# Optimization experiments

Measured on AMD Instinct MI355X. Metric: run time of the kernel, lower is better.

Reference implementation:

```python
import jax, jax.numpy as jnp
import numpy as np

V, E, H, O, L = 32000, 512, 512, 32, 2
B, T = 64, 512


def setup_inputs() -> dict:
    key = jax.random.key(0)
    ks = jax.random.split(key, 10)
    s = 0.02
    x = jax.random.randint(ks[0], (B, T), 0, V, dtype=jnp.int64)
    seq_lens = jax.random.randint(ks[1], (B,), 1, T + 1, dtype=jnp.int64)
    emb = jax.random.normal(ks[2], (V, E), dtype=jnp.float32) * s
    Whx = jax.random.normal(ks[3], (L, H, E), dtype=jnp.float32) * s  # [out,in] like nn.Linear
    Whh = jax.random.normal(ks[4], (L, H, H), dtype=jnp.float32) * s
    b_h = jnp.zeros((L, H), dtype=jnp.float32)
    Wyh = jax.random.normal(ks[5], (L, H, H), dtype=jnp.float32) * s
    b_y = jnp.zeros((L, H), dtype=jnp.float32)
    Wf = jax.random.normal(ks[6], (O, H), dtype=jnp.float32) * s
    bf = jnp.zeros((O,), dtype=jnp.float32)
    return {"x": x, "sequence_lengths": seq_lens, "emb": emb, "Whx": Whx,
            "Whh": Whh, "b_h": b_h, "Wyh": Wyh, "b_y": b_y, "Wf": Wf, "bf": bf}


def reference(x, sequence_lengths, emb, Whx, Whh, b_h, Wyh, b_y, Wf, bf):
    Bsz, Tlen = x.shape
    x_emb = emb[x]                      # [B,T,E]
    xs = jnp.swapaxes(x_emb, 0, 1)      # time-major [T,B,E]
    h0 = jnp.zeros((L, Bsz, H), dtype=x_emb.dtype)

    def step(h, xt):
        inp = xt
        hs = []
        for l in range(L):
            hl = jnp.tanh(inp @ Whx[l].T + h[l] @ Whh[l].T + b_h[l])
            hs.append(hl)
            inp = hl
        # only the last layer's y is kept by the original loop
        y = inp @ Wyh[L - 1].T + b_y[L - 1]
        return jnp.stack(hs), y

    _, outputs = jax.lax.scan(step, h0, xs)     # outputs: [T,B,H]
    outputs = jnp.swapaxes(outputs, 0, 1)       # [B,T,H]
    idx = sequence_lengths - 1                  # last valid timestep per example
    final_hidden = outputs[jnp.arange(Bsz), idx]  # [B,H]
    return final_hidden @ Wf.T + bf             # [B,O]
```

## Files before the change

kernel.cpp:

```cpp
#include <hip/hip_runtime.h>

namespace {
constexpr int E_ = 512;
constexpr int H_ = 512;
constexpr int O_ = 32;
constexpr int B_ = 64;
constexpr int T_ = 512;
constexpr int RING = 8;
constexpr int FPAD = 16;
constexpr size_t H0_OFF   = 0;
constexpr size_t H1_OFF   = (size_t)RING * B_ * H_;
constexpr size_t HF_OFF   = 2 * H1_OFF;
constexpr size_t FLAG_OFF = HF_OFF + (size_t)B_ * H_;
constexpr size_t FLAG_UINTS = 2u * 8u * 32u * FPAD;
constexpr size_t WS_REQUIRED = (FLAG_OFF + FLAG_UINTS) * 4;
}

typedef float f32x4 __attribute__((ext_vector_type(4)));

__device__ __forceinline__ void coh_ld2k(const float* p, f32x4& a, f32x4& b) {
    asm volatile(
        "global_load_dwordx4 %0, %2, off sc0 sc1\n\t"
        "global_load_dwordx4 %1, %2, off offset:1024 sc0 sc1\n\t"
        "s_waitcnt vmcnt(0)"
        : "=&v"(a), "=&v"(b) : "v"(p) : "memory");
}
__device__ __forceinline__ void coh_ld4k(const float* p, const float* q,
                                         f32x4& a, f32x4& b, f32x4& c, f32x4& d) {
    asm volatile(
        "global_load_dwordx4 %0, %4, off sc0 sc1\n\t"
        "global_load_dwordx4 %1, %4, off offset:1024 sc0 sc1\n\t"
        "global_load_dwordx4 %2, %5, off sc0 sc1\n\t"
        "global_load_dwordx4 %3, %5, off offset:1024 sc0 sc1\n\t"
        "s_waitcnt vmcnt(0)"
        : "=&v"(a), "=&v"(b), "=&v"(c), "=&v"(d) : "v"(p), "v"(q) : "memory");
}
__device__ __forceinline__ unsigned flag_poll(const unsigned* p) {
    unsigned v;
    asm volatile("global_load_dword %0, %1, off sc0 sc1\n\ts_waitcnt vmcnt(0)"
                 : "=&v"(v) : "v"(p) : "memory");
    return v;
}
__device__ __forceinline__ void vm_drain() {
    asm volatile("s_waitcnt vmcnt(0)" ::: "memory");
}
__device__ __forceinline__ void coh_store(float* p, float v) {
    asm volatile("global_store_dword %0, %1, off sc0 sc1" :: "v"(p), "v"(v) : "memory");
}
__device__ __forceinline__ void flag_store(unsigned* p, unsigned v) {
    asm volatile("global_store_dword %0, %1, off sc0 sc1" :: "v"(p), "v"(v) : "memory");
}

__device__ __forceinline__ float fast_tanh(float x) {
    float e = __builtin_amdgcn_exp2f(x * 2.885390081777927f);
    return 1.0f - 2.0f * __builtin_amdgcn_rcpf(e + 1.0f);
}

__device__ __forceinline__ float reduce4(const float v[4], int lane) {
    float a[2];
#pragma unroll
    for (int j = 0; j < 2; ++j) {
        const int sel = lane & 1;
        const float mine = sel ? v[2 * j + 1] : v[2 * j];
        const float send = sel ? v[2 * j] : v[2 * j + 1];
        a[j] = mine + __shfl_xor(send, 1, 64);
    }
    const int sel = (lane >> 1) & 1;
    const float mine = sel ? a[1] : a[0];
    const float send = sel ? a[0] : a[1];
    float s = mine + __shfl_xor(send, 2, 64);
    s += __shfl_xor(s, 4, 64);
    s += __shfl_xor(s, 8, 64);
    s += __shfl_xor(s, 16, 64);
    s += __shfl_xor(s, 32, 64);
    return s;
}

__global__ __launch_bounds__(512, 4) void rnn_pipe8(
    const int* __restrict__ x, const int* __restrict__ seq_lens,
    const float* __restrict__ emb,
    const float* __restrict__ Whx, const float* __restrict__ Whh,
    const float* __restrict__ b_h,
    float* __restrict__ h0_ring, float* __restrict__ h1_ring,
    float* __restrict__ h1_final, unsigned* __restrict__ flags)
{
    const int bid   = blockIdx.x;
    const int layer = bid >> 8;
    const int g     = (bid >> 5) & 7;
    const int c     = bid & 31;
    const int tid   = threadIdx.x;
    const int wid   = tid >> 6;
    const int lane  = tid & 63;
    const int we    = wid >> 2;
    const int wr    = wid & 3;
    const int rowbase = c * 16 + wr * 4;
    const int eg0   = g * 8 + we * 4;

    __shared__ float sx[2][4096];
    __shared__ float sh[4096];
    __shared__ float sh1[4096];

    const float* WxL = Whx + (size_t)layer * H_ * E_;
    const float* WhL = Whh + (size_t)layer * H_ * H_;
    f32x4 wx0[4], wx1[4], wh0[4], wh1[4];
#pragma unroll
    for (int r = 0; r < 4; ++r) {
        const int row = rowbase + r;
        wx0[r] = *(const f32x4*)(WxL + (size_t)row * E_ + (lane << 2));
        wx1[r] = *(const f32x4*)(WxL + (size_t)row * E_ + 256 + (lane << 2));
        wh0[r] = *(const f32x4*)(WhL + (size_t)row * H_ + (lane << 2));
        wh1[r] = *(const f32x4*)(WhL + (size_t)row * H_ + 256 + (lane << 2));
    }
    const float bias = b_h[layer * H_ + rowbase + (lane & 3)];

    int sl4[4];
#pragma unroll
    for (int q = 0; q < 4; ++q) sl4[q] = seq_lens[eg0 + q];
    int Tg = 1;
#pragma unroll
    for (int j = 0; j < 8; ++j) {
        const int s = seq_lens[g * 8 + j];
        Tg = s > Tg ? s : Tg;
    }

    unsigned* const myflag = flags + ((size_t)((layer * 8 + g) * 32 + c)) * FPAD;
    const unsigned* const pollp = (lane < 32)
        ? flags + ((size_t)(g * 32 + lane)) * FPAD
        : flags + ((size_t)((8 + g) * 32 + (lane - 32))) * FPAD;

    const int se  = wid;
    const int seg = g * 8 + se;

    long budget = 1l << 24;

    if (layer == 0) {
        {
            const int tok = x[(size_t)seg * T_];
            *(f32x4*)&sx[0][(se << 9) + (lane << 2)] =
                *(const f32x4*)(emb + ((size_t)tok << 9) + (lane << 2));
            *(f32x4*)&sx[0][(se << 9) + 256 + (lane << 2)] =
                *(const f32x4*)(emb + ((size_t)tok << 9) + 256 + (lane << 2));
        }
        __syncthreads();

        for (int t = 0; t < Tg; ++t) {
            const int cur = t & 1, slot = t & 7, pslot = (t - 1) & 7;
            float vvp[4][4];

#pragma unroll
            for (int q = 0; q < 4; ++q) {
                if (t >= sl4[q]) continue;
                const int el = (we << 2) + q;
                const f32x4 lx0 = *(const f32x4*)&sx[cur][(el << 9) + (lane << 2)];
                const f32x4 lx1 = *(const f32x4*)&sx[cur][(el << 9) + 256 + (lane << 2)];
#pragma unroll
                for (int r = 0; r < 4; ++r) {
                    float s = wx0[r][0] * lx0[0];
                    s = fmaf(wx0[r][1], lx0[1], s);
                    s = fmaf(wx0[r][2], lx0[2], s);
                    s = fmaf(wx0[r][3], lx0[3], s);
                    s = fmaf(wx1[r][0], lx1[0], s);
                    s = fmaf(wx1[r][1], lx1[1], s);
                    s = fmaf(wx1[r][2], lx1[2], s);
                    s = fmaf(wx1[r][3], lx1[3], s);
                    vvp[q][r] = s;
                }
            }
            f32x4 px0, px1;
            const bool havepf = (t + 1 < Tg);
            if (havepf) {
                const int tok = x[(size_t)seg * T_ + t + 1];
                px0 = *(const f32x4*)(emb + ((size_t)tok << 9) + (lane << 2));
                px1 = *(const f32x4*)(emb + ((size_t)tok << 9) + 256 + (lane << 2));
            }
            if (wid == 0 && t > 0) {
                const int tgt = (lane < 32) ? t : t - 7;
                for (;;) {
                    const unsigned v = flag_poll(pollp);
                    if (!__any((int)v < tgt)) break;
                    if (--budget < 0) break;
                }
            }
            __syncthreads();

            if (t > 0) {
                f32x4 a, b;
                coh_ld2k(h0_ring + (((size_t)pslot << 6) + seg) * 512 + (lane << 2), a, b);
                *(f32x4*)&sh[(se << 9) + (lane << 2)] = a;
                *(f32x4*)&sh[(se << 9) + 256 + (lane << 2)] = b;
            } else {
                f32x4 z = 0;
                *(f32x4*)&sh[(se << 9) + (lane << 2)] = z;
                *(f32x4*)&sh[(se << 9) + 256 + (lane << 2)] = z;
            }
            __syncthreads();

#pragma unroll
            for (int q = 0; q < 4; ++q) {
                if (t >= sl4[q]) continue;
                const int el = (we << 2) + q;
                const f32x4 h0a = *(const f32x4*)&sh[(el << 9) + (lane << 2)];
                const f32x4 h0b = *(const f32x4*)&sh[(el << 9) + 256 + (lane << 2)];
#pragma unroll
                for (int r = 0; r < 4; ++r) {
                    float s = vvp[q][r];
                    s = fmaf(wh0[r][0], h0a[0], s);
                    s = fmaf(wh0[r][1], h0a[1], s);
                    s = fmaf(wh0[r][2], h0a[2], s);
                    s = fmaf(wh0[r][3], h0a[3], s);
                    s = fmaf(wh1[r][0], h0b[0], s);
                    s = fmaf(wh1[r][1], h0b[1], s);
                    s = fmaf(wh1[r][2], h0b[2], s);
                    s = fmaf(wh1[r][3], h0b[3], s);
                    vvp[q][r] = s;
                }
                const float sum = reduce4(vvp[q], lane);
                const float hv = fast_tanh(sum + bias);
                if (lane < 4)
                    coh_store(h0_ring + (((size_t)slot << 6) + eg0 + q) * 512 + rowbase + lane, hv);
            }
            if (havepf) {
                *(f32x4*)&sx[cur ^ 1][(se << 9) + (lane << 2)] = px0;
                *(f32x4*)&sx[cur ^ 1][(se << 9) + 256 + (lane << 2)] = px1;
            }
            vm_drain();
            __syncthreads();
            if (tid == 0) flag_store(myflag, (unsigned)(t + 1));
        }
    } else {
        for (int t = 0; t < Tg; ++t) {
            const int slot = t & 7, pslot = (t - 1) & 7;
            float vvp[4][4];

            if (wid == 0) {
                const int tgt = (lane < 32) ? t + 1 : t;
                for (;;) {
                    const unsigned v = flag_poll(pollp);
                    if (!__any((int)v < tgt)) break;
                    if (--budget < 0) break;
                }
            }
            __syncthreads();

            if (t > 0) {
                f32x4 a, b, cc, d;
                coh_ld4k(h0_ring + (((size_t)slot << 6) + seg) * 512 + (lane << 2),
                         h1_ring + (((size_t)pslot << 6) + seg) * 512 + (lane << 2),
                         a, b, cc, d);
                *(f32x4*)&sh[(se << 9) + (lane << 2)] = a;
                *(f32x4*)&sh[(se << 9) + 256 + (lane << 2)] = b;
                *(f32x4*)&sh1[(se << 9) + (lane << 2)] = cc;
                *(f32x4*)&sh1[(se << 9) + 256 + (lane << 2)] = d;
            } else {
                f32x4 a, b;
                coh_ld2k(h0_ring + (((size_t)slot << 6) + seg) * 512 + (lane << 2), a, b);
                *(f32x4*)&sh[(se << 9) + (lane << 2)] = a;
                *(f32x4*)&sh[(se << 9) + 256 + (lane << 2)] = b;
                f32x4 z = 0;
                *(f32x4*)&sh1[(se << 9) + (lane << 2)] = z;
                *(f32x4*)&sh1[(se << 9) + 256 + (lane << 2)] = z;
            }
            __syncthreads();

#pragma unroll
            for (int q = 0; q < 4; ++q) {
                if (t >= sl4[q]) continue;
                const int el = (we << 2) + q;
                const f32x4 xa = *(const f32x4*)&sh[(el << 9) + (lane << 2)];
                const f32x4 xb = *(const f32x4*)&sh[(el << 9) + 256 + (lane << 2)];
                const f32x4 ha = *(const f32x4*)&sh1[(el << 9) + (lane << 2)];
                const f32x4 hb = *(const f32x4*)&sh1[(el << 9) + 256 + (lane << 2)];
#pragma unroll
                for (int r = 0; r < 4; ++r) {
                    float s = wx0[r][0] * xa[0];
                    s = fmaf(wx0[r][1], xa[1], s);
                    s = fmaf(wx0[r][2], xa[2], s);
                    s = fmaf(wx0[r][3], xa[3], s);
                    s = fmaf(wx1[r][0], xb[0], s);
                    s = fmaf(wx1[r][1], xb[1], s);
                    s = fmaf(wx1[r][2], xb[2], s);
                    s = fmaf(wx1[r][3], xb[3], s);
                    s = fmaf(wh0[r][0], ha[0], s);
                    s = fmaf(wh0[r][1], ha[1], s);
                    s = fmaf(wh0[r][2], ha[2], s);
                    s = fmaf(wh0[r][3], ha[3], s);
                    s = fmaf(wh1[r][0], hb[0], s);
                    s = fmaf(wh1[r][1], hb[1], s);
                    s = fmaf(wh1[r][2], hb[2], s);
                    s = fmaf(wh1[r][3], hb[3], s);
                    vvp[q][r] = s;
                }
                const float sum = reduce4(vvp[q], lane);
                const float hv = fast_tanh(sum + bias);
                if (lane < 4) {
                    coh_store(h1_ring + (((size_t)slot << 6) + eg0 + q) * 512 + rowbase + lane, hv);
                    if (t == sl4[q] - 1)
                        h1_final[((size_t)(eg0 + q) << 9) + rowbase + lane] = hv;
                }
            }
            vm_drain();
            __syncthreads();
            if (tid == 0) flag_store(myflag, (unsigned)(t + 1));
        }
    }
}

__device__ __forceinline__ float dot4(float4 a, float4 b) {
    return fmaf(a.x, b.x, fmaf(a.y, b.y, fmaf(a.z, b.z, a.w * b.w)));
}
__device__ __forceinline__ float wave_reduce(float acc) {
#pragma unroll
    for (int off = 32; off > 0; off >>= 1) acc += __shfl_down(acc, off, 64);
    return acc;
}

__global__ __launch_bounds__(512) void head_kernel(
    const float* __restrict__ h1f, const float* __restrict__ Wyh,
    const float* __restrict__ b_y, const float* __restrict__ Wf,
    const float* __restrict__ bf, float* __restrict__ out)
{
    const int e = blockIdx.x;
    const int tid = threadIdx.x, wid = tid >> 6, lane = tid & 63;
    const int k0 = lane << 3;
    __shared__ float sh[H_];
    __shared__ float sy[H_];
    sh[tid] = h1f[(size_t)e * H_ + tid];
    __syncthreads();
    const float4 hA = *(const float4*)&sh[k0];
    const float4 hB = *(const float4*)&sh[k0 + 4];
    const float* Wy1 = Wyh + H_ * H_;
#pragma unroll 4
    for (int rr = 0; rr < 64; ++rr) {
        const int row = (wid << 6) + rr;
        float acc = wave_reduce(dot4(*(const float4*)&Wy1[(size_t)row * H_ + k0], hA) +
                                dot4(*(const float4*)&Wy1[(size_t)row * H_ + k0 + 4], hB));
        if (lane == 0) sy[row] = acc + b_y[H_ + row];
    }
    __syncthreads();
    const float4 yA = *(const float4*)&sy[k0];
    const float4 yB = *(const float4*)&sy[k0 + 4];
#pragma unroll
    for (int rr = 0; rr < 4; ++rr) {
        const int o = (wid << 2) + rr;
        float acc = wave_reduce(dot4(*(const float4*)&Wf[(size_t)o * H_ + k0], yA) +
                                dot4(*(const float4*)&Wf[(size_t)o * H_ + k0 + 4], yB));
        if (lane == 0) out[(size_t)e * O_ + o] = acc + bf[o];
    }
}

__global__ __launch_bounds__(1024, 1) void rnn_fused_fb(
    const int* __restrict__ x, const int* __restrict__ seq_lens,
    const float* __restrict__ emb, const float* __restrict__ Whx,
    const float* __restrict__ Whh, const float* __restrict__ b_h,
    const float* __restrict__ Wyh, const float* __restrict__ b_y,
    const float* __restrict__ Wf, const float* __restrict__ bf,
    float* __restrict__ out)
{
    const int b = blockIdx.x, tid = threadIdx.x;
    const int wave = tid >> 6, lane = tid & 63, k0 = lane << 3;
    __shared__ float s_inp[E_];
    __shared__ float s_h0[2][H_];
    __shared__ float s_h1[2][H_];
    __shared__ float s_y[H_];
    if (tid < H_) { s_h0[0][tid]=0.f; s_h0[1][tid]=0.f; s_h1[0][tid]=0.f; s_h1[1][tid]=0.f; }
    const int Tb = seq_lens[b];
    const float* Whx0 = Whx; const float* Whx1 = Whx + H_*E_;
    const float* Whh0 = Whh; const float* Whh1 = Whh + H_*H_;
    for (int t = 0; t < Tb; ++t) {
        const int cur = t & 1, prv = cur ^ 1;
        if (tid < E_) { const int tok = x[b*T_+t]; s_inp[tid] = emb[(size_t)tok*E_+tid]; }
        __syncthreads();
        const float4 iA = *(const float4*)&s_inp[k0], iB = *(const float4*)&s_inp[k0+4];
        const float4 pA = *(const float4*)&s_h0[prv][k0], pB = *(const float4*)&s_h0[prv][k0+4];
#pragma unroll 4
        for (int r = 0; r < 32; ++r) {
            const int i = (wave<<5)+r;
            float acc = dot4(*(const float4*)&Whx0[i*E_+k0], iA) + dot4(*(const float4*)&Whx0[i*E_+k0+4], iB)
                      + dot4(*(const float4*)&Whh0[i*H_+k0], pA) + dot4(*(const float4*)&Whh0[i*H_+k0+4], pB);
            acc = wave_reduce(acc);
            if (lane == 0) s_h0[cur][i] = tanhf(acc + b_h[i]);
        }
        __syncthreads();
        const float4 cA = *(const float4*)&s_h0[cur][k0], cB = *(const float4*)&s_h0[cur][k0+4];
        const float4 qA = *(const float4*)&s_h1[prv][k0], qB = *(const float4*)&s_h1[prv][k0+4];
#pragma unroll 4
        for (int r = 0; r < 32; ++r) {
            const int i = (wave<<5)+r;
            float acc = dot4(*(const float4*)&Whx1[i*E_+k0], cA) + dot4(*(const float4*)&Whx1[i*E_+k0+4], cB)
                      + dot4(*(const float4*)&Whh1[i*H_+k0], qA) + dot4(*(const float4*)&Whh1[i*H_+k0+4], qB);
            acc = wave_reduce(acc);
            if (lane == 0) s_h1[cur][i] = tanhf(acc + b_h[H_+i]);
        }
        __syncthreads();
    }
    const int lastb = (Tb-1) & 1;
    const float4 hA = *(const float4*)&s_h1[lastb][k0], hB = *(const float4*)&s_h1[lastb][k0+4];
    const float* Wy1 = Wyh + H_*H_;
#pragma unroll 4
    for (int r = 0; r < 32; ++r) {
        const int i = (wave<<5)+r;
        float acc = wave_reduce(dot4(*(const float4*)&Wy1[i*H_+k0], hA) + dot4(*(const float4*)&Wy1[i*H_+k0+4], hB));
        if (lane == 0) s_y[i] = acc + b_y[H_+i];
    }
    __syncthreads();
    const float4 yA = *(const float4*)&s_y[k0], yB = *(const float4*)&s_y[k0+4];
    if (wave < 8) {
#pragma unroll
        for (int r = 0; r < 4; ++r) {
            const int o = (wave<<2)+r;
            float acc = wave_reduce(dot4(*(const float4*)&Wf[o*H_+k0], yA) + dot4(*(const float4*)&Wf[o*H_+k0+4], yB));
            if (lane == 0) out[b*O_+o] = acc + bf[o];
        }
    }
}

extern "C" void kernel_launch(void* const* d_in, const int* in_sizes, int n_in,
                              void* d_out, int out_size, void* d_ws, size_t ws_size,
                              hipStream_t stream) {
    const int*   x    = (const int*)d_in[0];
    const int*   sl   = (const int*)d_in[1];
    const float* emb  = (const float*)d_in[2];
    const float* Whx  = (const float*)d_in[3];
    const float* Whh  = (const float*)d_in[4];
    const float* b_h  = (const float*)d_in[5];
    const float* Wyh  = (const float*)d_in[6];
    const float* b_y  = (const float*)d_in[7];
    const float* Wf   = (const float*)d_in[8];
    const float* bf   = (const float*)d_in[9];
    float* out = (float*)d_out;

    if (ws_size < WS_REQUIRED) {
        rnn_fused_fb<<<B_, 1024, 0, stream>>>(x, sl, emb, Whx, Whh, b_h, Wyh, b_y, Wf, bf, out);
        return;
    }

    float* ws_f = (float*)d_ws;
    float* h0_ring = ws_f + H0_OFF;
    float* h1_ring = ws_f + H1_OFF;
    float* h1f     = ws_f + HF_OFF;
    unsigned* flags = (unsigned*)(ws_f + FLAG_OFF);

    hipMemsetAsync(flags, 0, FLAG_UINTS * sizeof(unsigned), stream);
    rnn_pipe8<<<512, 512, 0, stream>>>(x, sl, emb, Whx, Whh, b_h,
                                       h0_ring, h1_ring, h1f, flags);
    head_kernel<<<B_, 512, 0, stream>>>(h1f, Wyh, b_y, Wf, bf, out);
}
```

Measured before the change: 1.953 ms.

## Replace per-step flag handshakes with data-embedded validity via XOR epoch encoding

Data written to the ring buffers is XOR-encoded with a mask that flips every ring lap, so consumers detect fresh data by checking bit 30 of the loaded values and spin on the data itself instead of polling producer flags. Only layer-1 blocks publish flags, and layer 0 waits on them only for ring-slot reuse. This removes the store-drain and flag round-trip from the critical path of every step. Layer 0 now does its input and recurrent dot products together after the wait instead of overlapping the input part with it. It relies on valid tanh outputs never having bit 30 set after encoding, needs the rings pre-filled with 0xFF, and dead sequences must still write encoded values.

After: 1.941 ms (median of 2 runs). About the same (-0.6%).

```diff
diff --git a/kernel.cpp b/kernel.cpp
--- a/kernel.cpp
+++ b/kernel.cpp
@@ -12,7 +12,7 @@
 constexpr size_t H1_OFF   = (size_t)RING * B_ * H_;
 constexpr size_t HF_OFF   = 2 * H1_OFF;
 constexpr size_t FLAG_OFF = HF_OFF + (size_t)B_ * H_;
-constexpr size_t FLAG_UINTS = 2u * 8u * 32u * FPAD;
+constexpr size_t FLAG_UINTS = 8u * 32u * FPAD;
 constexpr size_t WS_REQUIRED = (FLAG_OFF + FLAG_UINTS) * 4;
 }
 
@@ -41,10 +41,7 @@
                  : "=&v"(v) : "v"(p) : "memory");
     return v;
 }
-__device__ __forceinline__ void vm_drain() {
-    asm volatile("s_waitcnt vmcnt(0)" ::: "memory");
-}
-__device__ __forceinline__ void coh_store(float* p, float v) {
+__device__ __forceinline__ void coh_store_u(float* p, unsigned v) {
     asm volatile("global_store_dword %0, %1, off sc0 sc1" :: "v"(p), "v"(v) : "memory");
 }
 __device__ __forceinline__ void flag_store(unsigned* p, unsigned v) {
@@ -76,7 +73,7 @@
     return s;
 }
 
-__global__ __launch_bounds__(512, 4) void rnn_pipe8(
+__global__ __launch_bounds__(512, 4) void rnn_pipe11(
     const int* __restrict__ x, const int* __restrict__ seq_lens,
     const float* __restrict__ emb,
     const float* __restrict__ Whx, const float* __restrict__ Whh,
@@ -96,9 +93,11 @@
     const int rowbase = c * 16 + wr * 4;
     const int eg0   = g * 8 + we * 4;
 
-    __shared__ float sx[2][4096];
-    __shared__ float sh[4096];
-    __shared__ float sh1[4096];
+    __shared__ float smem[12288];
+    float* const sxA = smem;
+    float* const sxB = smem + 4096;
+    float* const sh  = smem + 8192;
+    float* const sh1 = smem;
 
     const float* WxL = Whx + (size_t)layer * H_ * E_;
     const float* WhL = Whh + (size_t)layer * H_ * H_;
@@ -123,48 +122,62 @@
         Tg = s > Tg ? s : Tg;
     }
 
-    unsigned* const myflag = flags + ((size_t)((layer * 8 + g) * 32 + c)) * FPAD;
-    const unsigned* const pollp = (lane < 32)
-        ? flags + ((size_t)(g * 32 + lane)) * FPAD
-        : flags + ((size_t)((8 + g) * 32 + (lane - 32))) * FPAD;
+    unsigned* const myflag = flags + ((size_t)(g * 32 + c)) * FPAD;
+    const unsigned* const bp = flags + ((size_t)(g * 32 + (lane & 31))) * FPAD;
 
     const int se  = wid;
     const int seg = g * 8 + se;
 
-    long budget = 1l << 24;
+    long budget = 1l << 22;
 
     if (layer == 0) {
         {
             const int tok = x[(size_t)seg * T_];
-            *(f32x4*)&sx[0][(se << 9) + (lane << 2)] =
+            *(f32x4*)&sxA[(se << 9) + (lane << 2)] =
                 *(const f32x4*)(emb + ((size_t)tok << 9) + (lane << 2));
-            *(f32x4*)&sx[0][(se << 9) + 256 + (lane << 2)] =
+            *(f32x4*)&sxA[(se << 9) + 256 + (lane << 2)] =
                 *(const f32x4*)(emb + ((size_t)tok << 9) + 256 + (lane << 2));
         }
         __syncthreads();
 
         for (int t = 0; t < Tg; ++t) {
             const int cur = t & 1, slot = t & 7, pslot = (t - 1) & 7;
-            float vvp[4][4];
-
-#pragma unroll
-            for (int q = 0; q < 4; ++q) {
-                if (t >= sl4[q]) continue;
-                const int el = (we << 2) + q;
-                const f32x4 lx0 = *(const f32x4*)&sx[cur][(el << 9) + (lane << 2)];
-                const f32x4 lx1 = *(const f32x4*)&sx[cur][(el << 9) + 256 + (lane << 2)];
-#pragma unroll
-                for (int r = 0; r < 4; ++r) {
-                    float s = wx0[r][0] * lx0[0];
-                    s = fmaf(wx0[r][1], lx0[1], s);
-                    s = fmaf(wx0[r][2], lx0[2], s);
-                    s = fmaf(wx0[r][3], lx0[3], s);
-                    s = fmaf(wx1[r][0], lx1[0], s);
-                    s = fmaf(wx1[r][1], lx1[1], s);
-                    s = fmaf(wx1[r][2], lx1[2], s);
-                    s = fmaf(wx1[r][3], lx1[3], s);
-                    vvp[q][r] = s;
-                }
+            float* const sxc = cur ? sxB : sxA;
+            float* const sxn = cur ? sxA : sxB;
+            const unsigned em_prev = (((t - 1) >> 3) & 1) ? 0xFFFFFFFFu : 0u;
+            const unsigned em_cur  = ((t >> 3) & 1) ? 0xFFFFFFFFu : 0u;
+
+            if (wid == 0 && t >= RING) {
+                const int tgt = t - 7;
+                for (;;) {
+                    const unsigned v = flag_poll(bp);
+                    const bool bad = (lane < 32) && ((int)v < tgt);
+                    if (!__any(bad)) break;
+                    if (--budget < 0) break;
+                }
+            }
+
+            if (t > 0) {
+                const float* src = h0_ring + (((size_t)pslot << 6) + seg) * 512 + (lane << 2);
+                f32x4 da, db;
+                for (;;) {
+                    f32x4 a, b;
+                    coh_ld2k(src, a, b);
+                    unsigned o = 0;
+#pragma unroll
+                    for (int m = 0; m < 4; ++m) {
+                        unsigned u = __float_as_uint(a[m]) ^ em_prev; o |= u; da[m] = __uint_as_float(u);
+                        unsigned w = __float_as_uint(b[m]) ^ em_prev; o |= w; db[m] = __uint_as_float(w);
+                    }
+                    if (!__any((o >> 30) & 1)) break;
+                    if (--budget < 0) break;
+                }
+                *(f32x4*)&sh[(se << 9) + (lane << 2)] = da;
+                *(f32x4*)&sh[(se << 9) + 256 + (lane << 2)] = db;
+            } else {
+                f32x4 z = 0;
+                *(f32x4*)&sh[(se << 9) + (lane << 2)] = z;
+                *(f32x4*)&sh[(se << 9) + 256 + (lane << 2)] = z;
             }
             f32x4 px0, px1;
             const bool havepf = (t + 1 < Tg);
@@ -173,134 +186,145 @@
                 px0 = *(const f32x4*)(emb + ((size_t)tok << 9) + (lane << 2));
                 px1 = *(const f32x4*)(emb + ((size_t)tok << 9) + 256 + (lane << 2));
             }
-            if (wid == 0 && t > 0) {
-                const int tgt = (lane < 32) ? t : t - 7;
-                for (;;) {
-                    const unsigned v = flag_poll(pollp);
-                    if (!__any((int)v < tgt)) break;
-                    if (--budget < 0) break;
-                }
-            }
             __syncthreads();
 
-            if (t > 0) {
-                f32x4 a, b;
-                coh_ld2k(h0_ring + (((size_t)pslot << 6) + seg) * 512 + (lane << 2), a, b);
-                *(f32x4*)&sh[(se << 9) + (lane << 2)] = a;
-                *(f32x4*)&sh[(se << 9) + 256 + (lane << 2)] = b;
-            } else {
-                f32x4 z = 0;
-                *(f32x4*)&sh[(se << 9) + (lane << 2)] = z;
-                *(f32x4*)&sh[(se << 9) + 256 + (lane << 2)] = z;
+#pragma unroll
+            for (int q = 0; q < 4; ++q) {
+                unsigned uenc = em_cur;
+                if (t < sl4[q]) {
+                    const int el = (we << 2) + q;
+                    const f32x4 lx0 = *(const f32x4*)&sxc[(el << 9) + (lane << 2)];
+                    const f32x4 lx1 = *(const f32x4*)&sxc[(el << 9) + 256 + (lane << 2)];
+                    const f32x4 h0a = *(const f32x4*)&sh[(el << 9) + (lane << 2)];
+                    const f32x4 h0b = *(const f32x4*)&sh[(el << 9) + 256 + (lane << 2)];
+                    float vv[4];
+#pragma unroll
+                    for (int r = 0; r < 4; ++r) {
+                        float s = wx0[r][0] * lx0[0];
+                        s = fmaf(wx0[r][1], lx0[1], s);
+                        s = fmaf(wx0[r][2], lx0[2], s);
+                        s = fmaf(wx0[r][3], lx0[3], s);
+                        s = fmaf(wx1[r][0], lx1[0], s);
+                        s = fmaf(wx1[r][1], lx1[1], s);
+                        s = fmaf(wx1[r][2], lx1[2], s);
+                        s = fmaf(wx1[r][3], lx1[3], s);
+                        s = fmaf(wh0[r][0], h0a[0], s);
+                        s = fmaf(wh0[r][1], h0a[1], s);
+                        s = fmaf(wh0[r][2], h0a[2], s);
+                        s = fmaf(wh0[r][3], h0a[3], s);
+                        s = fmaf(wh1[r][0], h0b[0], s);
+                        s = fmaf(wh1[r][1], h0b[1], s);
+                        s = fmaf(wh1[r][2], h0b[2], s);
+                        s = fmaf(wh1[r][3], h0b[3], s);
+                        vv[r] = s;
+                    }
+                    const float sum = reduce4(vv, lane);
+                    const float hv = fast_tanh(sum + bias);
+                    uenc = __float_as_uint(hv) ^ em_cur;
+                }
+                if (lane < 4)
+                    coh_store_u(h0_ring + (((size_t)slot << 6) + eg0 + q) * 512 + rowbase + lane, uenc);
+            }
+            if (havepf) {
+                *(f32x4*)&sxn[(se << 9) + (lane << 2)] = px0;
+                *(f32x4*)&sxn[(se << 9) + 256 + (lane << 2)] = px1;
             }
             __syncthreads();
-
-#pragma unroll
-            for (int q = 0; q < 4; ++q) {
-                if (t >= sl4[q]) continue;
-                const int el = (we << 2) + q;
-                const f32x4 h0a = *(const f32x4*)&sh[(el << 9) + (lane << 2)];
-                const f32x4 h0b = *(const f32x4*)&sh[(el << 9) + 256 + (lane << 2)];
-#pragma unroll
-                for (int r = 0; r < 4; ++r) {
-                    float s = vvp[q][r];
-                    s = fmaf(wh0[r][0], h0a[0], s);
-                    s = fmaf(wh0[r][1], h0a[1], s);
-                    s = fmaf(wh0[r][2], h0a[2], s);
-                    s = fmaf(wh0[r][3], h0a[3], s);
-                    s = fmaf(wh1[r][0], h0b[0], s);
-                    s = fmaf(wh1[r][1], h0b[1], s);
-                    s = fmaf(wh1[r][2], h0b[2], s);
-                    s = fmaf(wh1[r][3], h0b[3], s);
-                    vvp[q][r] = s;
-                }
-                const float sum = reduce4(vvp[q], lane);
-                const float hv = fast_tanh(sum + bias);
-                if (lane < 4)
-                    coh_store(h0_ring + (((size_t)slot << 6) + eg0 + q) * 512 + rowbase + lane, hv);
-            }
-            if (havepf) {
-                *(f32x4*)&sx[cur ^ 1][(se << 9) + (lane << 2)] = px0;
-                *(f32x4*)&sx[cur ^ 1][(se << 9) + 256 + (lane << 2)] = px1;
-            }
-            vm_drain();
-            __syncthreads();
-            if (tid == 0) flag_store(myflag, (unsigned)(t + 1));
         }
     } else {
         for (int t = 0; t < Tg; ++t) {
             const int slot = t & 7, pslot = (t - 1) & 7;
-            float vvp[4][4];
-
-            if (wid == 0) {
-                const int tgt = (lane < 32) ? t + 1 : t;
+            const unsigned em0 = ((t >> 3) & 1) ? 0xFFFFFFFFu : 0u;
+            const unsigned em1 = (((t - 1) >> 3) & 1) ? 0xFFFFFFFFu : 0u;
+
+            const float* p0 = h0_ring + (((size_t)slot << 6) + seg) * 512 + (lane << 2);
+            if (t > 0) {
+                const float* p1 = h1_ring + (((size_t)pslot << 6) + seg) * 512 + (lane << 2);
+                f32x4 d0a, d0b, d1a, d1b;
                 for (;;) {
-                    const unsigned v = flag_poll(pollp);
-                    if (!__any((int)v < tgt)) break;
+                    f32x4 a, b, c2, d2;
+                    coh_ld4k(p0, p1, a, b, c2, d2);
+                    unsigned o = 0;
+#pragma unroll
+                    for (int m = 0; m < 4; ++m) {
+                        unsigned u0 = __float_as_uint(a[m])  ^ em0; o |= u0; d0a[m] = __uint_as_float(u0);
+                        unsigned u1 = __float_as_uint(b[m])  ^ em0; o |= u1; d0b[m] = __uint_as_float(u1);
+                        unsigned u2 = __float_as_uint(c2[m]) ^ em1; o |= u2; d1a[m] = __uint_as_float(u2);
+                        unsigned u3 = __float_as_uint(d2[m]) ^ em1; o |= u3; d1b[m] = __uint_as_float(u3);
+                    }
+                    if (!__any((o >> 30) & 1)) break;
                     if (--budget < 0) break;
                 }
-            }
-            __syncthreads();
-
-            if (t > 0) {
-                f32x4 a, b, cc, d;
-                coh_ld4k(h0_ring + (((size_t)slot << 6) + seg) * 512 + (lane << 2),
-                         h1_ring + (((size_t)pslot << 6) + seg) * 512 + (lane << 2),
-                         a, b, cc, d);
-                *(f32x4*)&sh[(se << 9) + (lane << 2)] = a;
-                *(f32x4*)&sh[(se << 9) + 256 + (lane << 2)] = b;
-                *(f32x4*)&sh1[(se << 9) + (lane << 2)] = cc;
-                *(f32x4*)&sh1[(se << 9) + 256 + (lane << 2)] = d;
+                *(f32x4*)&sh[(se << 9) + (lane << 2)] = d0a;
+                *(f32x4*)&sh[(se << 9) + 256 + (lane << 2)] = d0b;
+                *(f32x4*)&sh1[(se << 9) + (lane << 2)] = d1a;
+                *(f32x4*)&sh1[(se << 9) + 256 + (lane << 2)] = d1b;
             } else {
-                f32x4 a, b;
-                coh_ld2k(h0_ring + (((size_t)slot << 6) + seg) * 512 + (lane << 2), a, b);
-                *(f32x4*)&sh[(se << 9) + (lane << 2)] = a;
-                *(f32x4*)&sh[(se << 9) + 256 + (lane << 2)] = b;
+                f32x4 d0a, d0b;
+                for (;;) {
+                    f32x4 a, b;
+                    coh_ld2k(p0, a, b);
+                    unsigned o = 0;
+#pragma unroll
+                    for (int m = 0; m < 4; ++m) {
+                        unsigned u0 = __float_as_uint(a[m]) ^ em0; o |= u0; d0a[m] = __uint_as_float(u0);
+                        unsigned u1 = __float_as_uint(b[m]) ^ em0; o |= u1; d0b[m] = __uint_as_float(u1);
+                    }
+                    if (!__any((o >> 30) & 1)) break;
+                    if (--budget < 0) break;
+                }
+                *(f32x4*)&sh[(se << 9) + (lane << 2)] = d0a;
+                *(f32x4*)&sh[(se << 9) + 256 + (lane << 2)] = d0b;
                 f32x4 z = 0;
                 *(f32x4*)&sh1[(se << 9) + (lane << 2)] = z;
                 *(f32x4*)&sh1[(se << 9) + 256 + (lane << 2)] = z;
             }
             __syncthreads();
+            if (tid == 0) flag_store(myflag, (unsigned)(t + 1));
 
 #pragma unroll
             for (int q = 0; q < 4; ++q) {
-                if (t >= sl4[q]) continue;
-                const int el = (we << 2) + q;
-                const f32x4 xa = *(const f32x4*)&sh[(el << 9) + (lane << 2)];
-                const f32x4 xb = *(const f32x4*)&sh[(el << 9) + 256 + (lane << 2)];
-                const f32x4 ha = *(const f32x4*)&sh1[(el << 9) + (lane << 2)];
-                const f32x4 hb = *(const f32x4*)&sh1[(el << 9) + 256 + (lane << 2)];
-#pragma unroll
-                for (int r = 0; r < 4; ++r) {
-                    float s = wx0[r][0] * xa[0];
-                    s = fmaf(wx0[r][1], xa[1], s);
-                    s = fmaf(wx0[r][2], xa[2], s);
-                    s = fmaf(wx0[r][3], xa[3], s);
-                    s = fmaf(wx1[r][0], xb[0], s);
-                    s = fmaf(wx1[r][1], xb[1], s);
-                    s = fmaf(wx1[r][2], xb[2], s);
-                    s = fmaf(wx1[r][3], xb[3], s);
-                    s = fmaf(wh0[r][0], ha[0], s);
-                    s = fmaf(wh0[r][1], ha[1], s);
-                    s = fmaf(wh0[r][2], ha[2], s);
-                    s = fmaf(wh0[r][3], ha[3], s);
-                    s = fmaf(wh1[r][0], hb[0], s);
-                    s = fmaf(wh1[r][1], hb[1], s);
-                    s = fmaf(wh1[r][2], hb[2], s);
-                    s = fmaf(wh1[r][3], hb[3], s);
-                    vvp[q][r] = s;
-                }
-                const float sum = reduce4(vvp[q], lane);
-                const float hv = fast_tanh(sum + bias);
+                unsigned uenc = em0;
+                const bool live = (t < sl4[q]);
+                float hv = 0.f;
+                if (live) {
+                    const int el = (we << 2) + q;
+                    const f32x4 xa = *(const f32x4*)&sh[(el << 9) + (lane << 2)];
+                    const f32x4 xb = *(const f32x4*)&sh[(el << 9) + 256 + (lane << 2)];
+                    const f32x4 ha = *(const f32x4*)&sh1[(el << 9) + (lane << 2)];
+                    const f32x4 hb = *(const f32x4*)&sh1[(el << 9) + 256 + (lane << 2)];
+                    float vv[4];
+#pragma unroll
+                    for (int r = 0; r < 4; ++r) {
+                        float s = wx0[r][0] * xa[0];
+                        s = fmaf(wx0[r][1], xa[1], s);
+                        s = fmaf(wx0[r][2], xa[2], s);
+                        s = fmaf(wx0[r][3], xa[3], s);
+                        s = fmaf(wx1[r][0], xb[0], s);
+                        s = fmaf(wx1[r][1], xb[1], s);
+                        s = fmaf(wx1[r][2], xb[2], s);
+                        s = fmaf(wx1[r][3], xb[3], s);
+                        s = fmaf(wh0[r][0], ha[0], s);
+                        s = fmaf(wh0[r][1], ha[1], s);
+                        s = fmaf(wh0[r][2], ha[2], s);
+                        s = fmaf(wh0[r][3], ha[3], s);
+                        s = fmaf(wh1[r][0], hb[0], s);
+                        s = fmaf(wh1[r][1], hb[1], s);
+                        s = fmaf(wh1[r][2], hb[2], s);
+                        s = fmaf(wh1[r][3], hb[3], s);
+                        vv[r] = s;
+                    }
+                    const float sum = reduce4(vv, lane);
+                    hv = fast_tanh(sum + bias);
+                    uenc = __float_as_uint(hv) ^ em0;
+                }
                 if (lane < 4) {
-                    coh_store(h1_ring + (((size_t)slot << 6) + eg0 + q) * 512 + rowbase + lane, hv);
-                    if (t == sl4[q] - 1)
+                    coh_store_u(h1_ring + (((size_t)slot << 6) + eg0 + q) * 512 + rowbase + lane, uenc);
+                    if (live && t == sl4[q] - 1)
                         h1_final[((size_t)(eg0 + q) << 9) + rowbase + lane] = hv;
                 }
             }
-            vm_drain();
             __syncthreads();
-            if (tid == 0) flag_store(myflag, (unsigned)(t + 1));
         }
     }
 }
@@ -440,8 +464,9 @@
     float* h1f     = ws_f + HF_OFF;
     unsigned* flags = (unsigned*)(ws_f + FLAG_OFF);
 
+    hipMemsetAsync(h0_ring, 0xFF, 2 * H1_OFF * sizeof(float), stream);
     hipMemsetAsync(flags, 0, FLAG_UINTS * sizeof(unsigned), stream);
-    rnn_pipe8<<<512, 512, 0, stream>>>(x, sl, emb, Whx, Whh, b_h,
-                                       h0_ring, h1_ring, h1f, flags);
+    rnn_pipe11<<<512, 512, 0, stream>>>(x, sl, emb, Whx, Whh, b_h,
+                                        h0_ring, h1_ring, h1f, flags);
     head_kernel<<<B_, 512, 0, stream>>>(h1f, Wyh, b_y, Wf, bf, out);
 }
```
